# Kernel tuning notes

Hardware: AMD Instinct MI355X
Metric: run time of the kernel (lower is better)

## Reference

```python
import jax, jax.numpy as jnp
import numpy as np

N_ATOMS = 16384
N_SPECIES = 4
D_IN = 2880      # len(species)^2 * max_radial^2 * (max_angular+1) = 16*36*5
H = 256
N_STRUCTURES = 64


def setup_inputs() -> dict:
    key = jax.random.key(0)
    ks = jax.random.split(key, 9)
    features = jax.random.normal(ks[0], (N_ATOMS, D_IN), dtype=jnp.float32)
    # per-species MLP (MLPMap): 2 hidden layers with SiLU, then LinearMap -> 1
    w1 = jax.random.normal(ks[1], (N_SPECIES, D_IN, H), dtype=jnp.float32) * 0.02
    b1 = jax.random.normal(ks[2], (N_SPECIES, H), dtype=jnp.float32) * 0.02
    w2 = jax.random.normal(ks[3], (N_SPECIES, H, H), dtype=jnp.float32) * 0.05
    b2 = jax.random.normal(ks[4], (N_SPECIES, H), dtype=jnp.float32) * 0.02
    w_last = jax.random.normal(ks[5], (N_SPECIES, H), dtype=jnp.float32) * 0.05
    b_last = jax.random.normal(ks[6], (N_SPECIES,), dtype=jnp.float32) * 0.02
    comp_weights = jax.random.normal(ks[7], (N_SPECIES,), dtype=jnp.float32)
    # atoms are species-contiguous (TensorMap blocks); structures sorted
    structure_idx = jnp.sort(
        jax.random.randint(ks[8], (N_ATOMS,), 0, N_STRUCTURES, dtype=jnp.int32)
    )
    return {
        "features": features,
        "w1": w1, "b1": b1, "w2": w2, "b2": b2,
        "w_last": w_last, "b_last": b_last,
        "comp_weights": comp_weights,
        "structure_idx": structure_idx,
    }


def reference(features, w1, b1, w2, b2, w_last, b_last, comp_weights, structure_idx):
    S = N_SPECIES
    n_per = N_ATOMS // S
    # species-partitioned blocks: [S, n_per, D] — grouped GEMM form of the
    # per-species ModuleDict loop in MLPMap / LinearMap
    xs = features.reshape(S, n_per, D_IN)
    h = jax.nn.silu(jnp.einsum("snd,sdh->snh", xs, w1) + b1[:, None, :])
    h = jax.nn.silu(jnp.einsum("snh,shk->snk", h, w2) + b2[:, None, :])
    # LinearMap: per-species Linear(H, 1)
    e = jnp.einsum("snh,sh->sn", h, w_last) + b_last[:, None]  # [S, n_per]
    # apply_composition_contribution: add per-species composition weight
    species_per_atom = jnp.repeat(jnp.arange(S), n_per)
    atomic_energy = e.reshape(N_ATOMS) + comp_weights[species_per_atom]
    # keys_to_samples + sum_over_samples(['center','species_center'])
    total = jax.ops.segment_sum(atomic_energy, structure_idx,
                                num_segments=N_STRUCTURES)
    return total[:, None]  # [n_structures, 1] energy block
```

## Files before the change

### kernel.cpp

```cpp
#include <hip/hip_runtime.h>
#include <hip/hip_bf16.h>

#define D_IN    2880
#define HDIM    256
#define NSPEC   4
#define NATOMS  16384
#define NSTRUCT 64
#define BM      32
#define BK      64

typedef __attribute__((ext_vector_type(4))) float f32x4;
typedef __attribute__((ext_vector_type(8))) short s16x8;

__device__ __forceinline__ short f2bf(float f) {
    return (short)__builtin_bit_cast(unsigned short, __float2bfloat16(f));
}

template <int R, int C>
__global__ void xpose_bf16(const float* __restrict__ in, unsigned short* __restrict__ out) {
    __shared__ float tile[32][33];
    const int s  = blockIdx.z;
    const int r0 = blockIdx.x * 32;
    const int c0 = blockIdx.y * 32;
    const float* ip = in + (size_t)s * R * C;
    unsigned short* op = out + (size_t)s * C * R;
    const int tx = threadIdx.x, ty = threadIdx.y;
#pragma unroll
    for (int i = 0; i < 4; ++i)
        tile[ty + i * 8][tx] = ip[(size_t)(r0 + ty + i * 8) * C + (c0 + tx)];
    __syncthreads();
#pragma unroll
    for (int i = 0; i < 4; ++i)
        op[(size_t)(c0 + ty + i * 8) * R + (r0 + tx)] =
            (unsigned short)f2bf(tile[tx][ty + i * 8]);
}

__global__ __launch_bounds__(256, 2)
void fused_mlp(const float* __restrict__ feat,
               const unsigned short* __restrict__ w1t,
               const float* __restrict__ b1,
               const unsigned short* __restrict__ w2t,
               const float* __restrict__ b2,
               const float* __restrict__ w_last,
               const float* __restrict__ b_last,
               const float* __restrict__ comp_w,
               const int* __restrict__ sidx,
               float* __restrict__ out)
{
    __shared__ unsigned short As[BM][BK + 8];
    __shared__ unsigned short Bs[HDIM][BK + 8];
    __shared__ unsigned short H1[BM][HDIM + 8];
    __shared__ float ered[4][BM];

    const int tid  = threadIdx.x;
    const int lane = tid & 63;
    const int wv   = tid >> 6;
    const int lrow = lane & 15;
    const int lko  = (lane >> 4) * 8;
    const int lq   = lane >> 4;
    const int g    = blockIdx.x;
    const int row0 = g * BM;
    const int s    = g >> 7;

    const float* Ag = feat + (size_t)row0 * D_IN;
    const unsigned short* B1 = w1t + (size_t)s * HDIM * D_IN;

    f32x4 acc[2][4];
#pragma unroll
    for (int i = 0; i < 2; ++i)
#pragma unroll
        for (int j = 0; j < 4; ++j)
            acc[i][j] = (f32x4){0.f, 0.f, 0.f, 0.f};

    const int ar = tid >> 3;
    const int ac = tid & 7;

    for (int kt = 0; kt < D_IN / BK; ++kt) {
        const int k0 = kt * BK;
        {
            const float* ap = Ag + (size_t)ar * D_IN + k0 + ac * 8;
            f32x4 v0 = *(const f32x4*)ap;
            f32x4 v1 = *(const f32x4*)(ap + 4);
            s16x8 w;
            w[0] = f2bf(v0[0]); w[1] = f2bf(v0[1]); w[2] = f2bf(v0[2]); w[3] = f2bf(v0[3]);
            w[4] = f2bf(v1[0]); w[5] = f2bf(v1[1]); w[6] = f2bf(v1[2]); w[7] = f2bf(v1[3]);
            *(s16x8*)&As[ar][ac * 8] = w;
        }
        {
            const s16x8* bp = (const s16x8*)(B1 + (size_t)tid * D_IN + k0);
#pragma unroll
            for (int q = 0; q < 8; ++q)
                *(s16x8*)&Bs[tid][q * 8] = bp[q];
        }
        __syncthreads();
#pragma unroll
        for (int kk = 0; kk < 2; ++kk) {
            s16x8 af[2], bf_[4];
#pragma unroll
            for (int i = 0; i < 2; ++i)
                af[i] = *(const s16x8*)&As[i * 16 + lrow][kk * 32 + lko];
#pragma unroll
            for (int j = 0; j < 4; ++j)
                bf_[j] = *(const s16x8*)&Bs[wv * 64 + j * 16 + lrow][kk * 32 + lko];
#pragma unroll
            for (int i = 0; i < 2; ++i)
#pragma unroll
                for (int j = 0; j < 4; ++j)
                    acc[i][j] = __builtin_amdgcn_mfma_f32_16x16x32_bf16(
                        af[i], bf_[j], acc[i][j], 0, 0, 0);
        }
        __syncthreads();
    }

    {
        const float* b1s = b1 + s * HDIM;
#pragma unroll
        for (int j = 0; j < 4; ++j) {
            const int col = wv * 64 + j * 16 + lrow;
            const float bias = b1s[col];
#pragma unroll
            for (int i = 0; i < 2; ++i)
#pragma unroll
                for (int r = 0; r < 4; ++r) {
                    float x = acc[i][j][r] + bias;
                    float sg = 1.0f / (1.0f + __expf(-x));
                    H1[i * 16 + lq * 4 + r][col] = (unsigned short)f2bf(x * sg);
                }
        }
    }
#pragma unroll
    for (int i = 0; i < 2; ++i)
#pragma unroll
        for (int j = 0; j < 4; ++j)
            acc[i][j] = (f32x4){0.f, 0.f, 0.f, 0.f};

    const unsigned short* B2 = w2t + (size_t)s * HDIM * HDIM;
    for (int kt = 0; kt < HDIM / BK; ++kt) {
        const int k0 = kt * BK;
        {
            const s16x8* bp = (const s16x8*)(B2 + (size_t)tid * HDIM + k0);
#pragma unroll
            for (int q = 0; q < 8; ++q)
                *(s16x8*)&Bs[tid][q * 8] = bp[q];
        }
        __syncthreads();
#pragma unroll
        for (int kk = 0; kk < 2; ++kk) {
            s16x8 af[2], bf_[4];
#pragma unroll
            for (int i = 0; i < 2; ++i)
                af[i] = *(const s16x8*)&H1[i * 16 + lrow][k0 + kk * 32 + lko];
#pragma unroll
            for (int j = 0; j < 4; ++j)
                bf_[j] = *(const s16x8*)&Bs[wv * 64 + j * 16 + lrow][kk * 32 + lko];
#pragma unroll
            for (int i = 0; i < 2; ++i)
#pragma unroll
                for (int j = 0; j < 4; ++j)
                    acc[i][j] = __builtin_amdgcn_mfma_f32_16x16x32_bf16(
                        af[i], bf_[j], acc[i][j], 0, 0, 0);
        }
        __syncthreads();
    }

    {
        const float* b2s = b2 + s * HDIM;
        const float* wls = w_last + s * HDIM;
        float p[8];
#pragma unroll
        for (int t = 0; t < 8; ++t) p[t] = 0.f;
#pragma unroll
        for (int j = 0; j < 4; ++j) {
            const int col = wv * 64 + j * 16 + lrow;
            const float bias = b2s[col];
            const float wl = wls[col];
#pragma unroll
            for (int i = 0; i < 2; ++i)
#pragma unroll
                for (int r = 0; r < 4; ++r) {
                    float x = acc[i][j][r] + bias;
                    float sg = 1.0f / (1.0f + __expf(-x));
                    p[i * 4 + r] += x * sg * wl;
                }
        }
#pragma unroll
        for (int d = 1; d < 16; d <<= 1)
#pragma unroll
            for (int t = 0; t < 8; ++t)
                p[t] += __shfl_xor(p[t], d, 64);
        if (lrow == 0) {
#pragma unroll
            for (int i = 0; i < 2; ++i)
#pragma unroll
                for (int r = 0; r < 4; ++r)
                    ered[wv][i * 16 + lq * 4 + r] = p[i * 4 + r];
        }
        __syncthreads();
        if (tid < BM) {
            float e = ered[0][tid] + ered[1][tid] + ered[2][tid] + ered[3][tid]
                    + b_last[s] + comp_w[s];
            const int atom = row0 + tid;
            atomicAdd(&out[sidx[atom]], e);
        }
    }
}

extern "C" void kernel_launch(void* const* d_in, const int* in_sizes, int n_in,
                              void* d_out, int out_size, void* d_ws, size_t ws_size,
                              hipStream_t stream) {
    (void)in_sizes; (void)n_in; (void)out_size; (void)ws_size;
    const float* feat   = (const float*)d_in[0];
    const float* w1     = (const float*)d_in[1];
    const float* b1     = (const float*)d_in[2];
    const float* w2     = (const float*)d_in[3];
    const float* b2     = (const float*)d_in[4];
    const float* w_last = (const float*)d_in[5];
    const float* b_last = (const float*)d_in[6];
    const float* comp_w = (const float*)d_in[7];
    const int*   sidx   = (const int*)d_in[8];
    float* out = (float*)d_out;

    unsigned short* w1t = (unsigned short*)d_ws;
    unsigned short* w2t = (unsigned short*)((char*)d_ws + (size_t)NSPEC * HDIM * D_IN * 2);

    hipMemsetAsync(d_out, 0, NSTRUCT * sizeof(float), stream);
    xpose_bf16<D_IN, HDIM><<<dim3(D_IN / 32, HDIM / 32, NSPEC), dim3(32, 8), 0, stream>>>(w1, w1t);
    xpose_bf16<HDIM, HDIM><<<dim3(HDIM / 32, HDIM / 32, NSPEC), dim3(32, 8), 0, stream>>>(w2, w2t);
    fused_mlp<<<NATOMS / BM, 256, 0, stream>>>(feat, w1t, b1, w2t, b2,
                                               w_last, b_last, comp_w, sidx, out);
}
```

Measured before the change: 460.0 us.

## Prepack weights into MFMA fragment layout and double-buffer the fused MLP loop

Weights are pre-packed into bf16 tiles already laid out as MFMA B-fragments, so each wave loads its fragments straight from global memory into registers instead of staging them through shared memory. The activation tile is double-buffered in XOR-swizzled shared memory, and the next tile's loads are prefetched while the current MFMAs run. The block grows to 64 rows and 8 waves (2x4), and block indices are remapped so that species are interleaved. This should remove the shared-memory weight staging, bank conflicts and load stalls, at the cost of higher register pressure and redundant global weight reads across waves.

```diff
diff --git a/kernel.cpp b/kernel.cpp
--- a/kernel.cpp
+++ b/kernel.cpp
@@ -6,40 +6,61 @@
 #define NSPEC   4
 #define NATOMS  16384
 #define NSTRUCT 64
-#define BM      32
-#define BK      64
+#define NT1     45
+#define NT2     4
+#define BM      64
 
 typedef __attribute__((ext_vector_type(4))) float f32x4;
 typedef __attribute__((ext_vector_type(8))) short s16x8;
+typedef __attribute__((ext_vector_type(4))) unsigned short u16x4;
 
 __device__ __forceinline__ short f2bf(float f) {
     return (short)__builtin_bit_cast(unsigned short, __float2bfloat16(f));
 }
 
-template <int R, int C>
-__global__ void xpose_bf16(const float* __restrict__ in, unsigned short* __restrict__ out) {
-    __shared__ float tile[32][33];
-    const int s  = blockIdx.z;
-    const int r0 = blockIdx.x * 32;
-    const int c0 = blockIdx.y * 32;
-    const float* ip = in + (size_t)s * R * C;
-    unsigned short* op = out + (size_t)s * C * R;
-    const int tx = threadIdx.x, ty = threadIdx.y;
-#pragma unroll
-    for (int i = 0; i < 4; ++i)
-        tile[ty + i * 8][tx] = ip[(size_t)(r0 + ty + i * 8) * C + (c0 + tx)];
+template<int RDIM>
+__global__ void pack_w(const float* __restrict__ w, unsigned short* __restrict__ wp) {
+    __shared__ unsigned short T[64][264];
+    const int kt = blockIdx.x, s = blockIdx.y;
+    const int t = threadIdx.x;
+    const float* src = w + ((size_t)s * RDIM + kt * 64) * HDIM;
+#pragma unroll
+    for (int i = 0; i < 16; ++i) {
+        const int row = i * 4 + (t >> 6);
+        const int c4 = (t & 63) * 4;
+        f32x4 v = *(const f32x4*)(src + (size_t)row * HDIM + c4);
+        u16x4 u;
+        u[0] = (unsigned short)f2bf(v[0]); u[1] = (unsigned short)f2bf(v[1]);
+        u[2] = (unsigned short)f2bf(v[2]); u[3] = (unsigned short)f2bf(v[3]);
+        *(u16x4*)&T[row][c4] = u;
+    }
     __syncthreads();
-#pragma unroll
-    for (int i = 0; i < 4; ++i)
-        op[(size_t)(c0 + ty + i * 8) * R + (r0 + tx)] =
-            (unsigned short)f2bf(tile[tx][ty + i * 8]);
-}
-
-__global__ __launch_bounds__(256, 2)
+    unsigned short* dst = wp + ((size_t)s * (RDIM / 64) + kt) * 16384;
+    const int l = t & 63;
+#pragma unroll
+    for (int it = 0; it < 8; ++it) {
+        const int c = (t >> 6) + it * 4;
+        const int hq = c >> 1, kk = c & 1;
+        s16x8 vv;
+#pragma unroll
+        for (int e = 0; e < 8; ++e)
+            vv[e] = (short)T[kk * 32 + (l >> 4) * 8 + e][hq * 16 + (l & 15)];
+        *(s16x8*)(dst + (size_t)c * 512 + l * 8) = vv;
+    }
+}
+
+__device__ __forceinline__ int aswz(int row, int colbyte) {
+    return row * 128 + (colbyte ^ ((row & 7) << 4));
+}
+__device__ __forceinline__ int hswz(int row, int colbyte) {
+    return row * 512 + (colbyte ^ ((row & 7) << 4));
+}
+
+__global__ __launch_bounds__(512, 2)
 void fused_mlp(const float* __restrict__ feat,
-               const unsigned short* __restrict__ w1t,
+               const unsigned short* __restrict__ w1p,
                const float* __restrict__ b1,
-               const unsigned short* __restrict__ w2t,
+               const unsigned short* __restrict__ w2p,
                const float* __restrict__ b2,
                const float* __restrict__ w_last,
                const float* __restrict__ b_last,
@@ -47,67 +68,84 @@
                const int* __restrict__ sidx,
                float* __restrict__ out)
 {
-    __shared__ unsigned short As[BM][BK + 8];
-    __shared__ unsigned short Bs[HDIM][BK + 8];
-    __shared__ unsigned short H1[BM][HDIM + 8];
+    __shared__ __align__(16) char Ab[2][8192];
+    __shared__ __align__(16) char Hb[BM * 512];
     __shared__ float ered[4][BM];
 
     const int tid  = threadIdx.x;
     const int lane = tid & 63;
     const int wv   = tid >> 6;
-    const int lrow = lane & 15;
-    const int lko  = (lane >> 4) * 8;
-    const int lq   = lane >> 4;
+    const int wr   = wv >> 2, wc = wv & 3;
+    const int lrow = lane & 15, lq = lane >> 4;
     const int g    = blockIdx.x;
-    const int row0 = g * BM;
-    const int s    = g >> 7;
+    const int s    = (g & 7) >> 1;
+    const int mloc = ((g >> 3) << 1) | (g & 1);
+    const int row0 = s * (NATOMS / NSPEC) + mloc * BM;
 
     const float* Ag = feat + (size_t)row0 * D_IN;
-    const unsigned short* B1 = w1t + (size_t)s * HDIM * D_IN;
+    const unsigned short* B1 = w1p + (size_t)s * NT1 * 16384;
+    const unsigned short* B2 = w2p + (size_t)s * NT2 * 16384;
+
+    const int ar  = tid >> 3;
+    const int acb = (tid & 7) * 16;
+    const int awo = aswz(ar, acb);
 
     f32x4 acc[2][4];
 #pragma unroll
     for (int i = 0; i < 2; ++i)
 #pragma unroll
-        for (int j = 0; j < 4; ++j)
-            acc[i][j] = (f32x4){0.f, 0.f, 0.f, 0.f};
-
-    const int ar = tid >> 3;
-    const int ac = tid & 7;
-
-    for (int kt = 0; kt < D_IN / BK; ++kt) {
-        const int k0 = kt * BK;
-        {
-            const float* ap = Ag + (size_t)ar * D_IN + k0 + ac * 8;
-            f32x4 v0 = *(const f32x4*)ap;
-            f32x4 v1 = *(const f32x4*)(ap + 4);
-            s16x8 w;
-            w[0] = f2bf(v0[0]); w[1] = f2bf(v0[1]); w[2] = f2bf(v0[2]); w[3] = f2bf(v0[3]);
-            w[4] = f2bf(v1[0]); w[5] = f2bf(v1[1]); w[6] = f2bf(v1[2]); w[7] = f2bf(v1[3]);
-            *(s16x8*)&As[ar][ac * 8] = w;
-        }
-        {
-            const s16x8* bp = (const s16x8*)(B1 + (size_t)tid * D_IN + k0);
-#pragma unroll
-            for (int q = 0; q < 8; ++q)
-                *(s16x8*)&Bs[tid][q * 8] = bp[q];
-        }
-        __syncthreads();
-#pragma unroll
-        for (int kk = 0; kk < 2; ++kk) {
-            s16x8 af[2], bf_[4];
-#pragma unroll
-            for (int i = 0; i < 2; ++i)
-                af[i] = *(const s16x8*)&As[i * 16 + lrow][kk * 32 + lko];
+        for (int j = 0; j < 4; ++j) acc[i][j] = (f32x4){0.f, 0.f, 0.f, 0.f};
+
+    {
+        const float* ap = Ag + (size_t)ar * D_IN + (tid & 7) * 8;
+        f32x4 v0 = *(const f32x4*)ap;
+        f32x4 v1 = *(const f32x4*)(ap + 4);
+        s16x8 pw;
+        pw[0]=f2bf(v0[0]); pw[1]=f2bf(v0[1]); pw[2]=f2bf(v0[2]); pw[3]=f2bf(v0[3]);
+        pw[4]=f2bf(v1[0]); pw[5]=f2bf(v1[1]); pw[6]=f2bf(v1[2]); pw[7]=f2bf(v1[3]);
+        *(s16x8*)(&Ab[0][0] + awo) = pw;
+    }
+    s16x8 Bf[2][4][2];
+#pragma unroll
+    for (int j = 0; j < 4; ++j)
+#pragma unroll
+        for (int kk = 0; kk < 2; ++kk)
+            Bf[0][j][kk] = *(const s16x8*)(B1 + ((wc * 4 + j) * 2 + kk) * 512 + lane * 8);
+    __syncthreads();
+
+#pragma unroll 2
+    for (int kt = 0; kt < NT1; ++kt) {
+        const int cb = kt & 1, nb = cb ^ 1;
+        const bool hn = (kt + 1) < NT1;
+        f32x4 a0, a1;
+        if (hn) {
+            const float* ap = Ag + (size_t)ar * D_IN + (kt + 1) * 64 + (tid & 7) * 8;
+            a0 = *(const f32x4*)ap;
+            a1 = *(const f32x4*)(ap + 4);
 #pragma unroll
             for (int j = 0; j < 4; ++j)
-                bf_[j] = *(const s16x8*)&Bs[wv * 64 + j * 16 + lrow][kk * 32 + lko];
+#pragma unroll
+                for (int kk = 0; kk < 2; ++kk)
+                    Bf[nb][j][kk] = *(const s16x8*)(B1 + ((size_t)(kt + 1) * 32 + (wc * 4 + j) * 2 + kk) * 512 + lane * 8);
+        }
+        s16x8 af[2][2];
+#pragma unroll
+        for (int i = 0; i < 2; ++i)
+#pragma unroll
+            for (int kk = 0; kk < 2; ++kk)
+                af[i][kk] = *(const s16x8*)(&Ab[cb][0] + aswz(wr * 32 + i * 16 + lrow, kk * 64 + lq * 16));
+#pragma unroll
+        for (int kk = 0; kk < 2; ++kk)
 #pragma unroll
             for (int i = 0; i < 2; ++i)
 #pragma unroll
                 for (int j = 0; j < 4; ++j)
-                    acc[i][j] = __builtin_amdgcn_mfma_f32_16x16x32_bf16(
-                        af[i], bf_[j], acc[i][j], 0, 0, 0);
+                    acc[i][j] = __builtin_amdgcn_mfma_f32_16x16x32_bf16(af[i][kk], Bf[cb][j][kk], acc[i][j], 0, 0, 0);
+        if (hn) {
+            s16x8 pw;
+            pw[0]=f2bf(a0[0]); pw[1]=f2bf(a0[1]); pw[2]=f2bf(a0[2]); pw[3]=f2bf(a0[3]);
+            pw[4]=f2bf(a1[0]); pw[5]=f2bf(a1[1]); pw[6]=f2bf(a1[2]); pw[7]=f2bf(a1[3]);
+            *(s16x8*)(&Ab[nb][0] + awo) = pw;
         }
         __syncthreads();
     }
@@ -116,7 +154,7 @@
         const float* b1s = b1 + s * HDIM;
 #pragma unroll
         for (int j = 0; j < 4; ++j) {
-            const int col = wv * 64 + j * 16 + lrow;
+            const int col = wc * 64 + j * 16 + lrow;
             const float bias = b1s[col];
 #pragma unroll
             for (int i = 0; i < 2; ++i)
@@ -124,43 +162,47 @@
                 for (int r = 0; r < 4; ++r) {
                     float x = acc[i][j][r] + bias;
                     float sg = 1.0f / (1.0f + __expf(-x));
-                    H1[i * 16 + lq * 4 + r][col] = (unsigned short)f2bf(x * sg);
+                    const int row = wr * 32 + i * 16 + lq * 4 + r;
+                    *(unsigned short*)(&Hb[0] + hswz(row, col * 2)) = (unsigned short)f2bf(x * sg);
                 }
         }
     }
 #pragma unroll
     for (int i = 0; i < 2; ++i)
 #pragma unroll
-        for (int j = 0; j < 4; ++j)
-            acc[i][j] = (f32x4){0.f, 0.f, 0.f, 0.f};
-
-    const unsigned short* B2 = w2t + (size_t)s * HDIM * HDIM;
-    for (int kt = 0; kt < HDIM / BK; ++kt) {
-        const int k0 = kt * BK;
-        {
-            const s16x8* bp = (const s16x8*)(B2 + (size_t)tid * HDIM + k0);
-#pragma unroll
-            for (int q = 0; q < 8; ++q)
-                *(s16x8*)&Bs[tid][q * 8] = bp[q];
-        }
-        __syncthreads();
-#pragma unroll
-        for (int kk = 0; kk < 2; ++kk) {
-            s16x8 af[2], bf_[4];
-#pragma unroll
-            for (int i = 0; i < 2; ++i)
-                af[i] = *(const s16x8*)&H1[i * 16 + lrow][k0 + kk * 32 + lko];
+        for (int j = 0; j < 4; ++j) acc[i][j] = (f32x4){0.f, 0.f, 0.f, 0.f};
+
+    s16x8 B2f[2][4][2];
+#pragma unroll
+    for (int j = 0; j < 4; ++j)
+#pragma unroll
+        for (int kk = 0; kk < 2; ++kk)
+            B2f[0][j][kk] = *(const s16x8*)(B2 + ((wc * 4 + j) * 2 + kk) * 512 + lane * 8);
+    __syncthreads();
+
+#pragma unroll
+    for (int kt = 0; kt < NT2; ++kt) {
+        const int cb = kt & 1, nb = cb ^ 1;
+        if (kt + 1 < NT2) {
 #pragma unroll
             for (int j = 0; j < 4; ++j)
-                bf_[j] = *(const s16x8*)&Bs[wv * 64 + j * 16 + lrow][kk * 32 + lko];
+#pragma unroll
+                for (int kk = 0; kk < 2; ++kk)
+                    B2f[nb][j][kk] = *(const s16x8*)(B2 + ((size_t)(kt + 1) * 32 + (wc * 4 + j) * 2 + kk) * 512 + lane * 8);
+        }
+        s16x8 af[2][2];
+#pragma unroll
+        for (int i = 0; i < 2; ++i)
+#pragma unroll
+            for (int kk = 0; kk < 2; ++kk)
+                af[i][kk] = *(const s16x8*)(&Hb[0] + hswz(wr * 32 + i * 16 + lrow, kt * 128 + kk * 64 + lq * 16));
+#pragma unroll
+        for (int kk = 0; kk < 2; ++kk)
 #pragma unroll
             for (int i = 0; i < 2; ++i)
 #pragma unroll
                 for (int j = 0; j < 4; ++j)
-                    acc[i][j] = __builtin_amdgcn_mfma_f32_16x16x32_bf16(
-                        af[i], bf_[j], acc[i][j], 0, 0, 0);
-        }
-        __syncthreads();
+                    acc[i][j] = __builtin_amdgcn_mfma_f32_16x16x32_bf16(af[i][kk], B2f[cb][j][kk], acc[i][j], 0, 0, 0);
     }
 
     {
@@ -171,7 +213,7 @@
         for (int t = 0; t < 8; ++t) p[t] = 0.f;
 #pragma unroll
         for (int j = 0; j < 4; ++j) {
-            const int col = wv * 64 + j * 16 + lrow;
+            const int col = wc * 64 + j * 16 + lrow;
             const float bias = b2s[col];
             const float wl = wls[col];
 #pragma unroll
@@ -193,14 +235,13 @@
             for (int i = 0; i < 2; ++i)
 #pragma unroll
                 for (int r = 0; r < 4; ++r)
-                    ered[wv][i * 16 + lq * 4 + r] = p[i * 4 + r];
+                    ered[wc][wr * 32 + i * 16 + lq * 4 + r] = p[i * 4 + r];
         }
         __syncthreads();
         if (tid < BM) {
             float e = ered[0][tid] + ered[1][tid] + ered[2][tid] + ered[3][tid]
                     + b_last[s] + comp_w[s];
-            const int atom = row0 + tid;
-            atomicAdd(&out[sidx[atom]], e);
+            atomicAdd(&out[sidx[row0 + tid]], e);
         }
     }
 }
@@ -220,12 +261,12 @@
     const int*   sidx   = (const int*)d_in[8];
     float* out = (float*)d_out;
 
-    unsigned short* w1t = (unsigned short*)d_ws;
-    unsigned short* w2t = (unsigned short*)((char*)d_ws + (size_t)NSPEC * HDIM * D_IN * 2);
+    unsigned short* w1p = (unsigned short*)d_ws;
+    unsigned short* w2p = w1p + (size_t)NSPEC * NT1 * 16384;
 
     hipMemsetAsync(d_out, 0, NSTRUCT * sizeof(float), stream);
-    xpose_bf16<D_IN, HDIM><<<dim3(D_IN / 32, HDIM / 32, NSPEC), dim3(32, 8), 0, stream>>>(w1, w1t);
-    xpose_bf16<HDIM, HDIM><<<dim3(HDIM / 32, HDIM / 32, NSPEC), dim3(32, 8), 0, stream>>>(w2, w2t);
-    fused_mlp<<<NATOMS / BM, 256, 0, stream>>>(feat, w1t, b1, w2t, b2,
-                                               w_last, b_last, comp_w, sidx, out);
-}
+    pack_w<D_IN><<<dim3(NT1, NSPEC), 256, 0, stream>>>(w1, w1p);
+    pack_w<HDIM><<<dim3(NT2, NSPEC), 256, 0, stream>>>(w2, w2p);
+    fused_mlp<<<256, 512, 0, stream>>>(feat, w1p, b1, w2p, b2,
+                                       w_last, b_last, comp_w, sidx, out);
+}
```

Result: faster. 403.9 us (-12.2%).
